# Performance work log

Measured on AMD Instinct MI355X. Metric: run time of the kernel, lower is better.

Reference implementation:

```python
import jax, jax.numpy as jnp
import numpy as np

B, S, N = 16, 512, 8          # batch, sentence length, num hash functions
M_BLOOM = 4096                # bloom filter length
W_WIN = 2                     # moving-window half width


def setup_inputs() -> dict:
    key = jax.random.key(0)
    hashes = jax.random.randint(key, (B, S, N), 0, 2147483647, dtype=jnp.int32)
    return {"hashes": hashes}


def counting_bloom(hashes, m):
    # hashes: [B, S, N] int -> counts [B, M, S] float32 (per-position histogram of N hashes mod m)
    b, s, _ = hashes.shape
    fp = jnp.remainder(hashes, m)
    counts = jnp.zeros((b, s, m), jnp.float32).at[
        jnp.arange(b)[:, None, None], jnp.arange(s)[None, :, None], fp
    ].add(1.0)
    return jnp.transpose(counts, (0, 2, 1))  # [B, M, S]


def moving_window(fc, w):
    # fc: [B, M, S] -> [B, (2w+1)*M, S]; block k holds fc shifted right by (w-k) along S, zero-padded
    _, _, s = fc.shape
    blocks = []
    for k in range(2 * w + 1):
        sh = w - k  # positive = shift right, negative = shift left
        if sh > 0:
            blk = jnp.pad(fc[:, :, : s - sh], ((0, 0), (0, 0), (sh, 0)))
        elif sh < 0:
            blk = jnp.pad(fc[:, :, -sh:], ((0, 0), (0, 0), (0, -sh)))
        else:
            blk = fc
        blocks.append(blk)
    return jnp.concatenate(blocks, axis=1)


def reference(hashes):
    fc = counting_bloom(hashes, M_BLOOM)      # [B, M, S]
    return moving_window(fc, W_WIN)           # [B, (2W+1)*M, S]
```

## Files before the change

### kernel.cpp

```cpp
#include <hip/hip_runtime.h>
#include <stdint.h>

#define B_DIM 16
#define S_DIM 512
#define N_HASH 8
#define M_BLOOM 4096
#define W_WIN 2
#define K_BLOCKS (2 * W_WIN + 1)
#define OUT_ELEMS (B_DIM * K_BLOCKS * M_BLOOM * S_DIM)

#define M_CHUNK 64
#define TILE_STRIDE 520
#define TILE_BYTES (M_CHUNK * TILE_STRIDE)

typedef float fx4 __attribute__((ext_vector_type(4)));

__global__ __launch_bounds__(256) void bloom_window_kernel(
    const int* __restrict__ hashes, float* __restrict__ out) {
    __shared__ uint32_t tile32[TILE_BYTES / 4];
    uint8_t* tile = (uint8_t*)tile32;

    const int tid = threadIdx.x;
    const int b = blockIdx.x >> 6;
    const int chunk = blockIdx.x & 63;
    const int m0 = chunk * M_CHUNK;

    for (int i = tid; i < TILE_BYTES / 4; i += 256) tile32[i] = 0;
    __syncthreads();

    const int4* hp = (const int4*)hashes;
#pragma unroll
    for (int ss = 0; ss < 2; ++ss) {
        const int s = 2 * tid + ss;
        const int4 h01 = hp[(b * S_DIM + s) * 2 + 0];
        const int4 h23 = hp[(b * S_DIM + s) * 2 + 1];
        const int hv[8] = {h01.x, h01.y, h01.z, h01.w,
                           h23.x, h23.y, h23.z, h23.w};
#pragma unroll
        for (int n = 0; n < N_HASH; ++n) {
            const int m = hv[n] & (M_BLOOM - 1);
            const unsigned ml = (unsigned)(m - m0);
            if (ml < M_CHUNK) {
                tile[ml * TILE_STRIDE + 4 + s] += 1;
            }
        }
    }
    __syncthreads();

    fx4* out4 = (fx4*)out;
    const int n_items = K_BLOCKS * M_CHUNK * (S_DIM / 4);
    for (int idx = tid; idx < n_items; idx += 256) {
        const int j = idx & 127;
        const int r = idx >> 7;
        const int k = r >> 6;
        const int m = r & 63;

        const int base = m * TILE_STRIDE + 4 + 4 * j + (k - 2);
        const uint32_t* wp = (const uint32_t*)(tile + (base & ~3));
        const uint32_t lo = wp[0];
        const uint32_t hi = wp[1];
        const uint32_t sh = (uint32_t)(base & 3) * 8u;
        const uint32_t packed = sh ? ((lo >> sh) | (hi << (32u - sh))) : lo;

        fx4 v;
        v.x = (float)(packed & 0xffu);
        v.y = (float)((packed >> 8) & 0xffu);
        v.z = (float)((packed >> 16) & 0xffu);
        v.w = (float)((packed >> 24) & 0xffu);

        const int row = (b * K_BLOCKS + k) * M_BLOOM + m0 + m;
        out4[(long long)row * (S_DIM / 4) + j] = v;
    }
}

extern "C" void kernel_launch(void* const* d_in, const int* in_sizes, int n_in,
                              void* d_out, int out_size, void* d_ws, size_t ws_size,
                              hipStream_t stream) {
    const int* hashes = (const int*)d_in[0];
    float* out = (float*)d_out;

    bloom_window_kernel<<<B_DIM * (M_BLOOM / M_CHUNK), 256, 0, stream>>>(hashes, out);
}
```

Baseline: 653.1 us.

## Share tile word loads across five window shifts and use nontemporal output stores

New measurement: 650.5 us. No clear change (-0.4%).

```diff
diff --git a/kernel.cpp b/kernel.cpp
--- a/kernel.cpp
+++ b/kernel.cpp
@@ -17,7 +17,7 @@
 
 __global__ __launch_bounds__(256) void bloom_window_kernel(
     const int* __restrict__ hashes, float* __restrict__ out) {
-    __shared__ uint32_t tile32[TILE_BYTES / 4];
+    __shared__ __align__(16) uint32_t tile32[TILE_BYTES / 4];
     uint8_t* tile = (uint8_t*)tile32;
 
     const int tid = threadIdx.x;
@@ -25,7 +25,9 @@
     const int chunk = blockIdx.x & 63;
     const int m0 = chunk * M_CHUNK;
 
-    for (int i = tid; i < TILE_BYTES / 4; i += 256) tile32[i] = 0;
+    uint4* t4 = (uint4*)tile32;
+    for (int i = tid; i < TILE_BYTES / 16; i += 256)
+        t4[i] = make_uint4(0u, 0u, 0u, 0u);
     __syncthreads();
 
     const int4* hp = (const int4*)hashes;
@@ -47,29 +49,39 @@
     }
     __syncthreads();
 
+    const int j = tid & 127;
+    const int mb = tid >> 7;
     fx4* out4 = (fx4*)out;
-    const int n_items = K_BLOCKS * M_CHUNK * (S_DIM / 4);
-    for (int idx = tid; idx < n_items; idx += 256) {
-        const int j = idx & 127;
-        const int r = idx >> 7;
-        const int k = r >> 6;
-        const int m = r & 63;
 
-        const int base = m * TILE_STRIDE + 4 + 4 * j + (k - 2);
-        const uint32_t* wp = (const uint32_t*)(tile + (base & ~3));
-        const uint32_t lo = wp[0];
-        const uint32_t hi = wp[1];
-        const uint32_t sh = (uint32_t)(base & 3) * 8u;
-        const uint32_t packed = sh ? ((lo >> sh) | (hi << (32u - sh))) : lo;
+    const uint32_t* wp0 = tile32 + mb * (TILE_STRIDE / 4) + j;
+    const size_t obase0 =
+        ((size_t)(b * K_BLOCKS) * M_BLOOM + m0 + mb) * (S_DIM / 4) + j;
 
-        fx4 v;
-        v.x = (float)(packed & 0xffu);
-        v.y = (float)((packed >> 8) & 0xffu);
-        v.z = (float)((packed >> 16) & 0xffu);
-        v.w = (float)((packed >> 24) & 0xffu);
+#pragma unroll 4
+    for (int it = 0; it < M_CHUNK / 2; ++it) {
+        const uint32_t* wp = wp0 + it * (2 * TILE_STRIDE / 4);
+        const uint32_t w0 = wp[0];
+        const uint32_t w1 = wp[1];
+        const uint32_t w2 = wp[2];
+        const size_t ob = obase0 + (size_t)(2 * it) * (S_DIM / 4);
 
-        const int row = (b * K_BLOCKS + k) * M_BLOOM + m0 + m;
-        out4[(long long)row * (S_DIM / 4) + j] = v;
+        uint32_t p[K_BLOCKS];
+        p[0] = (w0 >> 16) | (w1 << 16);
+        p[1] = (w0 >> 24) | (w1 << 8);
+        p[2] = w1;
+        p[3] = (w1 >> 8) | (w2 << 24);
+        p[4] = (w1 >> 16) | (w2 << 16);
+
+#pragma unroll
+        for (int k = 0; k < K_BLOCKS; ++k) {
+            fx4 v;
+            v.x = (float)(p[k] & 0xffu);
+            v.y = (float)((p[k] >> 8) & 0xffu);
+            v.z = (float)((p[k] >> 16) & 0xffu);
+            v.w = (float)(p[k] >> 24);
+            __builtin_nontemporal_store(
+                v, &out4[ob + (size_t)k * (M_BLOOM * (S_DIM / 4))]);
+        }
     }
 }
 
```
